# Kernel tuning notes

Measured on AMD Instinct MI355X. Metric: run time of the kernel, lower is better.

Reference implementation:

```python
import jax, jax.numpy as jnp
import numpy as np

VOCAB = 1_000_000
B, F, E = 16384, 39, 16
LAYERS = [200, 200, 200]


def setup_inputs() -> dict:
    key = jax.random.key(0)
    ks = jax.random.split(key, 12)
    feat_ids = jax.random.randint(ks[0], (B, F), 0, VOCAB)
    feat_vals = jnp.ones((B, F), dtype=jnp.float32)
    # xavier-ish init for tables and MLP weights
    w = jax.random.normal(ks[1], (VOCAB, 1), dtype=jnp.float32) * 0.01
    v = jax.random.normal(ks[2], (VOCAB, E), dtype=jnp.float32) * 0.01
    b = jnp.zeros((1,), dtype=jnp.float32)
    params = {}
    node_in = E
    for i, h in enumerate(LAYERS):
        scale = (2.0 / (node_in + h)) ** 0.5
        params[f'w{i}'] = jax.random.normal(ks[3 + i], (node_in, h), dtype=jnp.float32) * scale
        params[f'b{i}'] = jnp.zeros((h,), dtype=jnp.float32)
        node_in = h
    return dict(feat_ids=feat_ids, feat_vals=feat_vals, w=w, v=v, b=b,
                w0=params['w0'], b0=params['b0'],
                w1=params['w1'], b1=params['b1'],
                w2=params['w2'], b2=params['b2'])


def reference(feat_ids, feat_vals, w, v, b, w0, b0, w1, b1, w2, b2):
    # X @ v  (sparse one-hot matmul == embedding gather + weighted sum over fields)
    ve = v[feat_ids]                                   # [B, F, E]
    xv = jnp.einsum('bf,bfe->be', feat_vals, ve)       # [B, E]
    # X^2 @ v^2
    x2v2 = jnp.einsum('bf,bfe->be', feat_vals * feat_vals, ve * ve)  # [B, E]
    fm = 0.5 * (xv * xv - x2v2)                        # [B, E]
    # MLP (dropout in test mode: keep_prob = 1 -> identity)
    h = jax.nn.relu(fm @ w0 + b0)
    h = jax.nn.relu(h @ w1 + b1)
    h = jax.nn.relu(h @ w2 + b2)
    bilinear = jnp.sum(h, axis=1, keepdims=True)       # [B, 1]
    # LR part: X @ w
    lr = jnp.einsum('bf,bfo->bo', feat_vals, w[feat_ids])  # [B, 1]
    logits = jnp.reshape(lr + b + bilinear, (-1,))     # [B]
    return jax.nn.sigmoid(logits)
```

## Files before the change

### kernel.cpp

```cpp
#include <hip/hip_runtime.h>
#include <math.h>

#define NFM_B 16384
#define NFM_F 39
#define NFM_E 16
#define NFM_H 200
#define TR    8
#define KPAD  232
#define NT    13
#define VOCAB 1000000
#define WSCALE  64.0f
#define WISCALE (1.0f / 64.0f)

typedef short short8   __attribute__((ext_vector_type(8)));
typedef short short4_t __attribute__((ext_vector_type(4)));
typedef float floatx4  __attribute__((ext_vector_type(4)));

__device__ __forceinline__ short f2bf(float x) {
    union { float f; unsigned u; } a; a.f = x;
    unsigned r = a.u + 0x7FFF + ((a.u >> 16) & 1);
    return (short)(r >> 16);
}

__device__ __forceinline__ unsigned char f_to_fp8(float x) {
    union { float f; unsigned u; } a; a.f = fabsf(x);
    const unsigned s = (x < 0.f) ? 0x80u : 0u;
    int e = (int)((a.u >> 23) & 255) - 127;
    if (a.f == 0.f) return (unsigned char)s;
    if (e < -6) {
        int m = (int)rintf(a.f * 512.f);
        if (m >= 8) return (unsigned char)(s | (1u << 3));
        return (unsigned char)(s | (unsigned)m);
    }
    unsigned m23 = a.u & 0x7FFFFF;
    unsigned m3  = m23 >> 20, rem = m23 & 0xFFFFF;
    if (rem > 0x80000 || (rem == 0x80000 && (m3 & 1))) m3++;
    if (m3 == 8) { m3 = 0; e++; }
    if (e > 8) { e = 8; m3 = 6; }
    return (unsigned char)(s | ((unsigned)(e + 7) << 3) | m3);
}
__device__ __forceinline__ float fp8_to_f(unsigned char b) {
    const unsigned s = (b >> 7) & 1, e = (b >> 3) & 15, m = b & 7;
    union { unsigned u; float f; } a;
    if (e == 0) {
        a.f = (float)m * 0.001953125f;
    } else {
        a.u = ((e - 7 + 127) << 23) | (m << 20);
    }
    if (s) a.f = -a.f;
    return a.f;
}

#define FRAG_OFF (VOCAB / 2)
#define W0F_OFF  0
#define W0F_SZ   (NT * 1 * 64 * 8)
#define W1F_OFF  (W0F_OFF + W0F_SZ)
#define W1F_SZ   (NT * 7 * 64 * 8)
#define W2F_OFF  (W1F_OFF + W1F_SZ)
#define W2F_SZ   (NT * 7 * 64 * 8)
#define WS_FRAGS (W2F_OFF + W2F_SZ)
#define FRAG_BLOCKS  ((WS_FRAGS + 255) / 256)
#define WCONV_THREADS (VOCAB / 8)
#define WCONV_BLOCKS ((WCONV_THREADS + 255) / 256)

__global__ __launch_bounds__(256)
void nfm_prep_kernel(const float* __restrict__ w,
                     const float* __restrict__ w0,
                     const float* __restrict__ w1,
                     const float* __restrict__ w2,
                     short* __restrict__ ws)
{
    if (blockIdx.x < FRAG_BLOCKS) {
        const int idx = blockIdx.x * 256 + threadIdx.x;
        if (idx >= WS_FRAGS) return;
        float val;
        if (idx < W1F_OFF) {
            const int rem = idx;
            const int j = rem & 7, lane = (rem >> 3) & 63, tile = rem >> 9;
            const int k = (lane >> 4) * 8 + j;
            const int n = tile * 16 + (lane & 15);
            val = (k < NFM_E && n < NFM_H) ? w0[k * NFM_H + n] : 0.f;
        } else if (idx < W2F_OFF) {
            const int rem = idx - W1F_OFF;
            const int j = rem & 7, lane = (rem >> 3) & 63;
            const int kt = rem >> 9;
            const int ks = kt % 7, tile = kt / 7;
            const int k = ks * 32 + (lane >> 4) * 8 + j;
            const int n = tile * 16 + (lane & 15);
            val = (k < NFM_H && n < NFM_H) ? w1[k * NFM_H + n] : 0.f;
        } else {
            const int rem = idx - W2F_OFF;
            const int j = rem & 7, lane = (rem >> 3) & 63;
            const int kt = rem >> 9;
            const int ks = kt % 7, tile = kt / 7;
            const int k = ks * 32 + (lane >> 4) * 8 + j;
            const int n = tile * 16 + (lane & 15);
            val = (k < NFM_H && n < NFM_H) ? w2[k * NFM_H + n] : 0.f;
        }
        ws[FRAG_OFF + idx] = f2bf(val);
    } else {
        const int t = (blockIdx.x - FRAG_BLOCKS) * 256 + threadIdx.x;
        if (t >= WCONV_THREADS) return;
        const int base = t * 8;
        const float4 a = *(const float4*)&w[base];
        const float4 b = *(const float4*)&w[base + 4];
        unsigned char o[8];
        o[0] = f_to_fp8(a.x * WSCALE); o[1] = f_to_fp8(a.y * WSCALE);
        o[2] = f_to_fp8(a.z * WSCALE); o[3] = f_to_fp8(a.w * WSCALE);
        o[4] = f_to_fp8(b.x * WSCALE); o[5] = f_to_fp8(b.y * WSCALE);
        o[6] = f_to_fp8(b.z * WSCALE); o[7] = f_to_fp8(b.w * WSCALE);
        *(uint2*)&((unsigned char*)ws)[base] = *(const uint2*)o;
    }
}

__global__ __launch_bounds__(256, 8)
void nfm_main_kernel(
    const int*   __restrict__ feat_ids,
    const float* __restrict__ feat_vals,
    const float* __restrict__ v,
    const float* __restrict__ bglob,
    const float* __restrict__ b0,
    const float* __restrict__ b1,
    const float* __restrict__ b2,
    const short* __restrict__ ws,
    float* __restrict__ out)
{
    __shared__ __attribute__((aligned(16))) short hbfA[16 * KPAD];
    __shared__ __attribute__((aligned(16))) short hbfB[16 * KPAD];
    __shared__ float rowsumW[4][16];
    __shared__ float lrS[TR];

    const int tid  = threadIdx.x;
    const int row0 = blockIdx.x * TR;
    const int lane = tid & 63;
    const int wv   = tid >> 6;
    const int lq   = lane >> 4;
    const int ln   = lane & 15;

    const unsigned char* w8  = (const unsigned char*)ws;
    const short*         Wfb = ws + FRAG_OFF;

    const int r8  = tid >> 5;
    const int l32 = tid & 31;
    const int fs  = l32 >> 2, eg = l32 & 3;
    const long rbase = (long)(row0 + r8) * NFM_F;

    int   idv[5]; float vlv[5];
#pragma unroll
    for (int it = 0; it < 5; ++it) {
        const int f = fs + it * 8;
        const bool ok = f < NFM_F;
        idv[it] = ok ? feat_ids [rbase + f] : 0;
        vlv[it] = ok ? feat_vals[rbase + f] : 0.f;
    }
    floatx4 ve[5];
#pragma unroll
    for (int it = 0; it < 5; ++it)
        ve[it] = __builtin_nontemporal_load(
                     (const floatx4*)&v[(long)idv[it] * NFM_E + eg * 4]);
    float lr = 0.f;
    if (eg == 0) {
#pragma unroll
        for (int it = 0; it < 5; ++it)
            lr += vlv[it] * fp8_to_f(w8[idv[it]]);
        lr *= WISCALE;
    }

    {
        short8 z8 = {0, 0, 0, 0, 0, 0, 0, 0};
        short8* pA = (short8*)hbfA;
        short8* pB = (short8*)hbfB;
        for (int i = tid; i < 464; i += 256) { pA[i] = z8; pB[i] = z8; }
    }
    __syncthreads();

    {
        floatx4 xv = {0.f, 0.f, 0.f, 0.f}, x2 = {0.f, 0.f, 0.f, 0.f};
#pragma unroll
        for (int it = 0; it < 5; ++it) {
            const float val = vlv[it];
            const float t0 = val * ve[it][0], t1 = val * ve[it][1];
            const float t2 = val * ve[it][2], t3 = val * ve[it][3];
            xv[0] += t0; xv[1] += t1; xv[2] += t2; xv[3] += t3;
            x2[0] = fmaf(t0, t0, x2[0]); x2[1] = fmaf(t1, t1, x2[1]);
            x2[2] = fmaf(t2, t2, x2[2]); x2[3] = fmaf(t3, t3, x2[3]);
        }
#pragma unroll
        for (int off = 4; off <= 16; off <<= 1) {
#pragma unroll
            for (int c = 0; c < 4; ++c) {
                xv[c] += __shfl_xor(xv[c], off, 32);
                x2[c] += __shfl_xor(x2[c], off, 32);
            }
        }
        if (fs == 0) {
            short4_t fm4;
#pragma unroll
            for (int c = 0; c < 4; ++c)
                fm4[c] = f2bf(0.5f * (xv[c] * xv[c] - x2[c]));
            *(short4_t*)&hbfB[r8 * KPAD + eg * 4] = fm4;
        }
#pragma unroll
        for (int off = 4; off <= 16; off <<= 1)
            lr += __shfl_xor(lr, off, 32);
        if (l32 == 0) lrS[r8] = lr;
    }
    __syncthreads();

    {
        const short8 af = *(const short8*)&hbfB[ln * KPAD + lq * 8];
        const short* Wf = Wfb + W0F_OFF;
        for (int t = wv; t < NT; t += 4) {
            const int n = t * 16 + ln;
            const float bj = (n < NFM_H) ? b0[n] : 0.f;
            floatx4 acc = {bj, bj, bj, bj};
            const short8 bf = *(const short8*)&Wf[(t * 64 + lane) * 8];
            acc = __builtin_amdgcn_mfma_f32_16x16x32_bf16(af, bf, acc, 0, 0, 0);
#pragma unroll
            for (int rg = 0; rg < 4; ++rg)
                hbfA[(lq * 4 + rg) * KPAD + n] = f2bf(fmaxf(acc[rg], 0.f));
        }
    }
    __syncthreads();

    {
        short8 af[7];
#pragma unroll
        for (int ks = 0; ks < 7; ++ks)
            af[ks] = *(const short8*)&hbfA[ln * KPAD + ks * 32 + lq * 8];
        const short* Wf = Wfb + W1F_OFF;
        for (int t = wv; t < NT; t += 4) {
            const int n = t * 16 + ln;
            const float bj = (n < NFM_H) ? b1[n] : 0.f;
            floatx4 acc = {bj, bj, bj, bj};
#pragma unroll
            for (int ks = 0; ks < 7; ++ks) {
                const short8 bf = *(const short8*)&Wf[((t * 7 + ks) * 64 + lane) * 8];
                acc = __builtin_amdgcn_mfma_f32_16x16x32_bf16(af[ks], bf, acc, 0, 0, 0);
            }
#pragma unroll
            for (int rg = 0; rg < 4; ++rg)
                hbfB[(lq * 4 + rg) * KPAD + n] = f2bf(fmaxf(acc[rg], 0.f));
        }
    }
    __syncthreads();

    {
        short8 af[7];
#pragma unroll
        for (int ks = 0; ks < 7; ++ks)
            af[ks] = *(const short8*)&hbfB[ln * KPAD + ks * 32 + lq * 8];
        const short* Wf = Wfb + W2F_OFF;
        float rs[4] = {0.f, 0.f, 0.f, 0.f};
        for (int t = wv; t < NT; t += 4) {
            const int n = t * 16 + ln;
            const float bj = (n < NFM_H) ? b2[n] : 0.f;
            floatx4 acc = {bj, bj, bj, bj};
#pragma unroll
            for (int ks = 0; ks < 7; ++ks) {
                const short8 bf = *(const short8*)&Wf[((t * 7 + ks) * 64 + lane) * 8];
                acc = __builtin_amdgcn_mfma_f32_16x16x32_bf16(af[ks], bf, acc, 0, 0, 0);
            }
#pragma unroll
            for (int rg = 0; rg < 4; ++rg)
                rs[rg] += fmaxf(acc[rg], 0.f);
        }
#pragma unroll
        for (int off = 8; off >= 1; off >>= 1)
#pragma unroll
            for (int rg = 0; rg < 4; ++rg)
                rs[rg] += __shfl_xor(rs[rg], off, 16);
        if (ln == 0)
#pragma unroll
            for (int rg = 0; rg < 4; ++rg)
                rowsumW[wv][lq * 4 + rg] = rs[rg];
    }
    __syncthreads();

    if (tid < TR) {
        const float s = rowsumW[0][tid] + rowsumW[1][tid]
                      + rowsumW[2][tid] + rowsumW[3][tid];
        const float logit = lrS[tid] + bglob[0] + s;
        out[row0 + tid] = 1.f / (1.f + expf(-logit));
    }
}

extern "C" void kernel_launch(void* const* d_in, const int* in_sizes, int n_in,
                              void* d_out, int out_size, void* d_ws, size_t ws_size,
                              hipStream_t stream) {
    const int*   feat_ids  = (const int*)  d_in[0];
    const float* feat_vals = (const float*)d_in[1];
    const float* w   = (const float*)d_in[2];
    const float* v   = (const float*)d_in[3];
    const float* b   = (const float*)d_in[4];
    const float* w0  = (const float*)d_in[5];
    const float* b0  = (const float*)d_in[6];
    const float* w1  = (const float*)d_in[7];
    const float* b1  = (const float*)d_in[8];
    const float* w2  = (const float*)d_in[9];
    const float* b2  = (const float*)d_in[10];
    float* out = (float*)d_out;
    short* ws  = (short*)d_ws;

    hipLaunchKernelGGL(nfm_prep_kernel, dim3(FRAG_BLOCKS + WCONV_BLOCKS), dim3(256),
                       0, stream, w, w0, w1, w2, ws);
    hipLaunchKernelGGL(nfm_main_kernel, dim3(NFM_B / TR), dim3(256), 0, stream,
                       feat_ids, feat_vals, v, b, b0, b1, b2, ws, out);
}
```

Measured before the change: 147.8 us.

## Quantize embedding table to fp8 in prep and gather 16-byte rows

The prep kernel now also converts the full embedding table v to scaled fp8 (e4m3) in the workspace. The main kernel gathers one 16-byte fp8 row per field and decodes it with hardware cvt builtins when available. The per-row reduction is remapped to one lane per field with 16-wide accumulators and a 5-level shuffle reduce, with the scale folded back in via FMSC. The aim is to shrink the random gather traffic, but every call now streams and rewrites the whole 1M×16 table, lowers embedding precision, and adds more shuffles.

```diff
diff --git a/kernel.cpp b/kernel.cpp
--- a/kernel.cpp
+++ b/kernel.cpp
@@ -11,10 +11,12 @@
 #define VOCAB 1000000
 #define WSCALE  64.0f
 #define WISCALE (1.0f / 64.0f)
+#define FMSC    (1.0f / 4096.0f)
 
 typedef short short8   __attribute__((ext_vector_type(8)));
 typedef short short4_t __attribute__((ext_vector_type(4)));
 typedef float floatx4  __attribute__((ext_vector_type(4)));
+typedef unsigned int uint4_t __attribute__((ext_vector_type(4)));
 
 __device__ __forceinline__ short f2bf(float x) {
     union { float f; unsigned u; } a; a.f = x;
@@ -39,19 +41,44 @@
     if (e > 8) { e = 8; m3 = 6; }
     return (unsigned char)(s | ((unsigned)(e + 7) << 3) | m3);
 }
-__device__ __forceinline__ float fp8_to_f(unsigned char b) {
+__device__ __forceinline__ float fp8_sw_decode(unsigned char b) {
     const unsigned s = (b >> 7) & 1, e = (b >> 3) & 15, m = b & 7;
     union { unsigned u; float f; } a;
-    if (e == 0) {
-        a.f = (float)m * 0.001953125f;
-    } else {
-        a.u = ((e - 7 + 127) << 23) | (m << 20);
-    }
+    if (e == 0) { a.f = (float)m * 0.001953125f; }
+    else        { a.u = ((e - 7 + 127) << 23) | (m << 20); }
     if (s) a.f = -a.f;
     return a.f;
 }
 
-#define FRAG_OFF (VOCAB / 2)
+#if defined(__has_builtin) && __has_builtin(__builtin_amdgcn_cvt_f32_fp8)
+__device__ __forceinline__ floatx4 cvt4_fp8(unsigned dw) {
+    floatx4 r;
+    r[0] = __builtin_amdgcn_cvt_f32_fp8((int)dw, 0);
+    r[1] = __builtin_amdgcn_cvt_f32_fp8((int)dw, 1);
+    r[2] = __builtin_amdgcn_cvt_f32_fp8((int)dw, 2);
+    r[3] = __builtin_amdgcn_cvt_f32_fp8((int)dw, 3);
+    return r;
+}
+__device__ __forceinline__ float cvt1_fp8(unsigned char b) {
+    return __builtin_amdgcn_cvt_f32_fp8((int)(unsigned)b, 0);
+}
+#else
+__device__ __forceinline__ floatx4 cvt4_fp8(unsigned dw) {
+    floatx4 r;
+    r[0] = fp8_sw_decode((unsigned char)(dw));
+    r[1] = fp8_sw_decode((unsigned char)(dw >> 8));
+    r[2] = fp8_sw_decode((unsigned char)(dw >> 16));
+    r[3] = fp8_sw_decode((unsigned char)(dw >> 24));
+    return r;
+}
+__device__ __forceinline__ float cvt1_fp8(unsigned char b) {
+    return fp8_sw_decode(b);
+}
+#endif
+
+#define V8_BYTES  (VOCAB * NFM_E)
+#define W8_BYTE_OFF V8_BYTES
+#define FRAG_BYTE_OFF (V8_BYTES + VOCAB)
 #define W0F_OFF  0
 #define W0F_SZ   (NT * 1 * 64 * 8)
 #define W1F_OFF  (W0F_OFF + W0F_SZ)
@@ -62,13 +89,16 @@
 #define FRAG_BLOCKS  ((WS_FRAGS + 255) / 256)
 #define WCONV_THREADS (VOCAB / 8)
 #define WCONV_BLOCKS ((WCONV_THREADS + 255) / 256)
+#define VCONV_THREADS (VOCAB * NFM_E / 8)
+#define VCONV_BLOCKS ((VCONV_THREADS + 255) / 256)
 
 __global__ __launch_bounds__(256)
-void nfm_prep_kernel(const float* __restrict__ w,
+void nfm_prep_kernel(const float* __restrict__ v,
+                     const float* __restrict__ w,
                      const float* __restrict__ w0,
                      const float* __restrict__ w1,
                      const float* __restrict__ w2,
-                     short* __restrict__ ws)
+                     unsigned char* __restrict__ wsb)
 {
     if (blockIdx.x < FRAG_BLOCKS) {
         const int idx = blockIdx.x * 256 + threadIdx.x;
@@ -97,8 +127,8 @@
             const int n = tile * 16 + (lane & 15);
             val = (k < NFM_H && n < NFM_H) ? w2[k * NFM_H + n] : 0.f;
         }
-        ws[FRAG_OFF + idx] = f2bf(val);
-    } else {
+        ((short*)(wsb + FRAG_BYTE_OFF))[idx] = f2bf(val);
+    } else if (blockIdx.x < FRAG_BLOCKS + WCONV_BLOCKS) {
         const int t = (blockIdx.x - FRAG_BLOCKS) * 256 + threadIdx.x;
         if (t >= WCONV_THREADS) return;
         const int base = t * 8;
@@ -109,7 +139,19 @@
         o[2] = f_to_fp8(a.z * WSCALE); o[3] = f_to_fp8(a.w * WSCALE);
         o[4] = f_to_fp8(b.x * WSCALE); o[5] = f_to_fp8(b.y * WSCALE);
         o[6] = f_to_fp8(b.z * WSCALE); o[7] = f_to_fp8(b.w * WSCALE);
-        *(uint2*)&((unsigned char*)ws)[base] = *(const uint2*)o;
+        *(uint2*)&wsb[W8_BYTE_OFF + base] = *(const uint2*)o;
+    } else {
+        const int t = (blockIdx.x - FRAG_BLOCKS - WCONV_BLOCKS) * 256 + threadIdx.x;
+        if (t >= VCONV_THREADS) return;
+        const long base = (long)t * 8;
+        const float4 a = *(const float4*)&v[base];
+        const float4 b = *(const float4*)&v[base + 4];
+        unsigned char o[8];
+        o[0] = f_to_fp8(a.x * WSCALE); o[1] = f_to_fp8(a.y * WSCALE);
+        o[2] = f_to_fp8(a.z * WSCALE); o[3] = f_to_fp8(a.w * WSCALE);
+        o[4] = f_to_fp8(b.x * WSCALE); o[5] = f_to_fp8(b.y * WSCALE);
+        o[6] = f_to_fp8(b.z * WSCALE); o[7] = f_to_fp8(b.w * WSCALE);
+        *(uint2*)&wsb[base] = *(const uint2*)o;
     }
 }
 
@@ -117,12 +159,11 @@
 void nfm_main_kernel(
     const int*   __restrict__ feat_ids,
     const float* __restrict__ feat_vals,
-    const float* __restrict__ v,
     const float* __restrict__ bglob,
     const float* __restrict__ b0,
     const float* __restrict__ b1,
     const float* __restrict__ b2,
-    const short* __restrict__ ws,
+    const unsigned char* __restrict__ wsb,
     float* __restrict__ out)
 {
     __shared__ __attribute__((aligned(16))) short hbfA[16 * KPAD];
@@ -137,34 +178,25 @@
     const int lq   = lane >> 4;
     const int ln   = lane & 15;
 
-    const unsigned char* w8  = (const unsigned char*)ws;
-    const short*         Wfb = ws + FRAG_OFF;
+    const unsigned char* v8  = wsb;
+    const unsigned char* w8  = wsb + W8_BYTE_OFF;
+    const short*         Wfb = (const short*)(wsb + FRAG_BYTE_OFF);
 
     const int r8  = tid >> 5;
     const int l32 = tid & 31;
-    const int fs  = l32 >> 2, eg = l32 & 3;
     const long rbase = (long)(row0 + r8) * NFM_F;
-
-    int   idv[5]; float vlv[5];
-#pragma unroll
-    for (int it = 0; it < 5; ++it) {
-        const int f = fs + it * 8;
-        const bool ok = f < NFM_F;
-        idv[it] = ok ? feat_ids [rbase + f] : 0;
-        vlv[it] = ok ? feat_vals[rbase + f] : 0.f;
-    }
-    floatx4 ve[5];
-#pragma unroll
-    for (int it = 0; it < 5; ++it)
-        ve[it] = __builtin_nontemporal_load(
-                     (const floatx4*)&v[(long)idv[it] * NFM_E + eg * 4]);
-    float lr = 0.f;
-    if (eg == 0) {
-#pragma unroll
-        for (int it = 0; it < 5; ++it)
-            lr += vlv[it] * fp8_to_f(w8[idv[it]]);
-        lr *= WISCALE;
-    }
+    const bool has2 = (l32 < 7);
+
+    const int   id1 = feat_ids [rbase + l32];
+    const float vl1 = feat_vals[rbase + l32];
+    int id2 = 0; float vl2 = 0.f;
+    if (has2) { id2 = feat_ids[rbase + 32 + l32]; vl2 = feat_vals[rbase + 32 + l32]; }
+
+    uint4_t r1 = __builtin_nontemporal_load((const uint4_t*)(v8 + (long)id1 * 16));
+    uint4_t r2 = {0u, 0u, 0u, 0u};
+    if (has2) r2 = __builtin_nontemporal_load((const uint4_t*)(v8 + (long)id2 * 16));
+    const unsigned char w1b = w8[id1];
+    const unsigned char w2b = has2 ? w8[id2] : (unsigned char)0;
 
     {
         short8 z8 = {0, 0, 0, 0, 0, 0, 0, 0};
@@ -175,35 +207,50 @@
     __syncthreads();
 
     {
-        floatx4 xv = {0.f, 0.f, 0.f, 0.f}, x2 = {0.f, 0.f, 0.f, 0.f};
-#pragma unroll
-        for (int it = 0; it < 5; ++it) {
-            const float val = vlv[it];
-            const float t0 = val * ve[it][0], t1 = val * ve[it][1];
-            const float t2 = val * ve[it][2], t3 = val * ve[it][3];
-            xv[0] += t0; xv[1] += t1; xv[2] += t2; xv[3] += t3;
-            x2[0] = fmaf(t0, t0, x2[0]); x2[1] = fmaf(t1, t1, x2[1]);
-            x2[2] = fmaf(t2, t2, x2[2]); x2[3] = fmaf(t3, t3, x2[3]);
-        }
-#pragma unroll
-        for (int off = 4; off <= 16; off <<= 1) {
+        float xv[16], x2[16];
+#pragma unroll
+        for (int e = 0; e < 16; ++e) { xv[e] = 0.f; x2[e] = 0.f; }
+#pragma unroll
+        for (int d = 0; d < 4; ++d) {
+            const floatx4 ve = cvt4_fp8(r1[d]);
+#pragma unroll
+            for (int s = 0; s < 4; ++s) {
+                const float t = vl1 * ve[s];
+                xv[d * 4 + s] += t;
+                x2[d * 4 + s] = fmaf(t, t, x2[d * 4 + s]);
+            }
+        }
+#pragma unroll
+        for (int d = 0; d < 4; ++d) {
+            const floatx4 ve = cvt4_fp8(r2[d]);
+#pragma unroll
+            for (int s = 0; s < 4; ++s) {
+                const float t = vl2 * ve[s];
+                xv[d * 4 + s] += t;
+                x2[d * 4 + s] = fmaf(t, t, x2[d * 4 + s]);
+            }
+        }
+        float lr = vl1 * cvt1_fp8(w1b) + vl2 * cvt1_fp8(w2b);
+
+#pragma unroll
+        for (int off = 1; off <= 16; off <<= 1) {
+#pragma unroll
+            for (int e = 0; e < 16; ++e) {
+                xv[e] += __shfl_xor(xv[e], off, 32);
+                x2[e] += __shfl_xor(x2[e], off, 32);
+            }
+            lr += __shfl_xor(lr, off, 32);
+        }
+        if (l32 < 4) {
+            short4_t fm4;
 #pragma unroll
             for (int c = 0; c < 4; ++c) {
-                xv[c] += __shfl_xor(xv[c], off, 32);
-                x2[c] += __shfl_xor(x2[c], off, 32);
-            }
-        }
-        if (fs == 0) {
-            short4_t fm4;
-#pragma unroll
-            for (int c = 0; c < 4; ++c)
-                fm4[c] = f2bf(0.5f * (xv[c] * xv[c] - x2[c]));
-            *(short4_t*)&hbfB[r8 * KPAD + eg * 4] = fm4;
-        }
-#pragma unroll
-        for (int off = 4; off <= 16; off <<= 1)
-            lr += __shfl_xor(lr, off, 32);
-        if (l32 == 0) lrS[r8] = lr;
+                const int e = l32 * 4 + c;
+                fm4[c] = f2bf(0.5f * (xv[e] * xv[e] - x2[e]) * FMSC);
+            }
+            *(short4_t*)&hbfB[r8 * KPAD + l32 * 4] = fm4;
+        }
+        if (l32 == 0) lrS[r8] = lr * WISCALE;
     }
     __syncthreads();
 
@@ -300,10 +347,11 @@
     const float* w2  = (const float*)d_in[9];
     const float* b2  = (const float*)d_in[10];
     float* out = (float*)d_out;
-    short* ws  = (short*)d_ws;
-
-    hipLaunchKernelGGL(nfm_prep_kernel, dim3(FRAG_BLOCKS + WCONV_BLOCKS), dim3(256),
-                       0, stream, w, w0, w1, w2, ws);
+    unsigned char* wsb = (unsigned char*)d_ws;
+
+    hipLaunchKernelGGL(nfm_prep_kernel,
+                       dim3(FRAG_BLOCKS + WCONV_BLOCKS + VCONV_BLOCKS), dim3(256),
+                       0, stream, v, w, w0, w1, w2, wsb);
     hipLaunchKernelGGL(nfm_main_kernel, dim3(NFM_B / TR), dim3(256), 0, stream,
-                       feat_ids, feat_vals, v, b, b0, b1, b2, ws, out);
-}
+                       feat_ids, feat_vals, b, b0, b1, b2, wsb, out);
+}
```

Result: slower. 179.5 us (+21.4%).
